# Kernel optimization log

Hardware: AMD Instinct MI355X
Metric: run time of the kernel (lower is better)

Reference implementation:

```python
import jax, jax.numpy as jnp
from jax import lax
import numpy as np

KW = 9
PAD = KW // 2  # 4, matches int(kernel_width/2) with stride-1 'same' conv


def _scnn_dir(x, w, b):
    """Sequential SCNN scan over axis 1 of x (shape [N, S, W, C]).
    Each step: cur = relu(conv1d_along_C(prev)) + x[:, i], out[0] = x[:, 0].
    conv is cross-correlation with kernel w (shape [KW]) + scalar bias b,
    matching nn.Conv2d(1, 1, kernel_size=(1, KW), padding=(0, PAD)).
    """
    k = w.reshape(1, 1, 1, KW)  # OIHW-style kernel: out=1, in=1, (1, KW)

    def conv(prev):  # prev: [N, W, C]
        y = lax.conv_general_dilated(prev[:, None, :, :], k,
                                     window_strides=(1, 1),
                                     padding=((0, 0), (PAD, PAD)))
        return y[:, 0] + b  # [N, W, C]

    xt = jnp.moveaxis(x, 1, 0)  # [S, N, W, C]

    def step(prev, xi):
        cur = jax.nn.relu(conv(prev)) + xi
        return cur, cur

    _, rest = lax.scan(step, xt[0], xt[1:])
    out = jnp.concatenate([xt[:1], rest], axis=0)
    return jnp.moveaxis(out, 0, 1)  # [N, S, W, C]


def setup_inputs() -> dict:
    key = jax.random.key(0)
    ks = jax.random.split(key, 9)
    N, C, H, W = 8, 128, 160, 160
    x = jax.random.normal(ks[0], (N, C, H, W), dtype=jnp.float32)
    scale = 1.0 / np.sqrt(KW)  # torch Conv2d default init scale (uniform bound)
    def wgt(k):
        return jax.random.uniform(k, (KW,), jnp.float32, -scale, scale)
    def bia(k):
        return jax.random.uniform(k, (), jnp.float32, -scale, scale)
    return {
        "x": x,
        "w_d": wgt(ks[1]), "b_d": bia(ks[2]),
        "w_u": wgt(ks[3]), "b_u": bia(ks[4]),
        "w_l": wgt(ks[5]), "b_l": bia(ks[6]),
        "w_r": wgt(ks[7]), "b_r": bia(ks[8]),
    }


def reference(x, w_d, b_d, w_u, b_u, w_l, b_l, w_r, b_r):
    out = jnp.transpose(x, (0, 2, 3, 1))                 # NCHW -> NHWC, scan over H (down)
    out = jax.nn.relu(_scnn_dir(out, w_d, b_d))
    out = jnp.flip(out, axis=1)                          # up direction
    out = jax.nn.relu(_scnn_dir(out, w_u, b_u))
    out = jnp.transpose(out, (0, 2, 1, 3))               # scan over W (left)
    out = jax.nn.relu(_scnn_dir(out, w_l, b_l))
    out = jnp.flip(out, axis=1)                          # right direction
    out = jax.nn.relu(_scnn_dir(out, w_r, b_r))
    return jnp.transpose(out, (0, 3, 2, 1))              # back to NCHW
```

## Files before the change

### kernel.cpp

```cpp
#include <hip/hip_runtime.h>

#define NB 8
#define CH 128
#define HH 160
#define WW 160
#define SPILL 100
#define LDS_ROWS 60

__device__ __forceinline__ float dpp_up1(float x) {
    return __int_as_float(__builtin_amdgcn_update_dpp(0, __float_as_int(x), 0x138, 0xF, 0xF, true));
}
__device__ __forceinline__ float dpp_dn1(float x) {
    return __int_as_float(__builtin_amdgcn_update_dpp(0, __float_as_int(x), 0x130, 0xF, 0xF, true));
}

__device__ __forceinline__ float2 conv9(float2 p, const float* w, float b) {
    float m1x = dpp_up1(p.x), m1y = dpp_up1(p.y);
    float m2x = dpp_up1(m1x), m2y = dpp_up1(m1y);
    float p1x = dpp_dn1(p.x), p1y = dpp_dn1(p.y);
    float p2x = dpp_dn1(p1x), p2y = dpp_dn1(p1y);
    float e0=m2x,e1=m2y,e2=m1x,e3=m1y,e4=p.x,e5=p.y,e6=p1x,e7=p1y,e8=p2x,e9=p2y;
    float ax = fmaf(w[0], e0, b);       ax = fmaf(w[3], e3, ax); ax = fmaf(w[6], e6, ax);
    float bx = w[1]*e1;                 bx = fmaf(w[4], e4, bx); bx = fmaf(w[7], e7, bx);
    float cx = w[2]*e2;                 cx = fmaf(w[5], e5, cx); cx = fmaf(w[8], e8, cx);
    float ay = fmaf(w[0], e1, b);       ay = fmaf(w[3], e4, ay); ay = fmaf(w[6], e7, ay);
    float by = w[1]*e2;                 by = fmaf(w[4], e5, by); by = fmaf(w[7], e8, by);
    float cy = w[2]*e3;                 cy = fmaf(w[5], e6, cy); cy = fmaf(w[8], e9, cy);
    return make_float2((ax + bx) + cx, (ay + by) + cy);
}

__global__ __launch_bounds__(256) void k0_transpose(const float* __restrict__ x,
                                                    float* __restrict__ A) {
    __shared__ float t[32][132];
    int p0 = blockIdx.x * 128;
    int c0 = blockIdx.y * 32;
    int n  = blockIdx.z;
    int tid = threadIdx.x;
    const float* xn = x + (size_t)n * CH * HH * WW;
    float* An = A + (size_t)n * HH * WW * CH;
    #pragma unroll
    for (int j = 0; j < 4; j++) {
        int c = j*8 + tid/32;
        int q4 = (tid%32)*4;
        float4 v = *(const float4*)(xn + (size_t)(c0 + c) * (HH*WW) + p0 + q4);
        *(float4*)&t[c][q4] = v;
    }
    __syncthreads();
    #pragma unroll
    for (int j = 0; j < 8; j++) {
        int p  = j*16 + tid/16;
        int cq = (tid%16)*2;
        float2 v = make_float2(t[cq][p], t[cq+1][p]);
        *(float2*)(An + (size_t)(p0 + p) * CH + c0 + cq) = v;
    }
}

__global__ __launch_bounds__(64) void k1_vert(float* __restrict__ A,
        const float* __restrict__ wdp, const float* __restrict__ bdp,
        const float* __restrict__ wup, const float* __restrict__ bup) {
    __shared__ float lds[LDS_ROWS][CH];
    int lane = threadIdx.x;
    int w = blockIdx.x, n = blockIdx.y;
    float wd[9], wu[9];
    #pragma unroll
    for (int j = 0; j < 9; j++) { wd[j] = wdp[j]; wu[j] = wup[j]; }
    float bd = bdp[0], bu = bup[0];
    float* col = A + ((size_t)n * HH * WW + w) * CH + 2*lane;
    const size_t RS = (size_t)WW * CH;

    float2 d;
    float2 qf[16];
    #pragma unroll
    for (int i = 0; i < 16; i++) qf[i] = *(const float2*)(col + (size_t)i * RS);
    for (int hb = 0; hb < HH; hb += 16) {
        #pragma unroll
        for (int k = 0; k < 16; k++) {
            int h = hb + k;
            float2 xr = qf[k];
            if (h + 16 < HH) qf[k] = *(const float2*)(col + (size_t)(h+16) * RS);
            if (h == 0) d = xr;
            else {
                float2 cv = conv9(d, wd, bd);
                d.x = fmaxf(cv.x, 0.f) + xr.x;
                d.y = fmaxf(cv.y, 0.f) + xr.y;
            }
            float rx = fmaxf(d.x, 0.f), ry = fmaxf(d.y, 0.f);
            if (h < SPILL) *(float2*)(col + (size_t)h * RS) = make_float2(rx, ry);
            else { lds[h-SPILL][lane] = rx; lds[h-SPILL][64+lane] = ry; }
        }
    }

    float2 u;
    float2 tf[8];
    #pragma unroll
    for (int k = 0; k < 8; k++) {
        int h = HH - 1 - k;
        tf[k] = make_float2(lds[h-SPILL][lane], lds[h-SPILL][64+lane]);
    }
    for (int sb = 0; sb < HH; sb += 8) {
        #pragma unroll
        for (int k = 0; k < 8; k++) {
            int s = sb + k;
            int h = HH - 1 - s;
            float2 t2 = tf[k];
            int h2 = h - 8;
            if (h2 >= SPILL)    tf[k] = make_float2(lds[h2-SPILL][lane], lds[h2-SPILL][64+lane]);
            else if (h2 >= 0)   tf[k] = *(const float2*)(col + (size_t)h2 * RS);
            if (s == 0) u = t2;
            else {
                float2 cv = conv9(u, wu, bu);
                u.x = fmaxf(cv.x, 0.f) + t2.x;
                u.y = fmaxf(cv.y, 0.f) + t2.y;
            }
            *(float2*)(col + (size_t)h * RS) = u;
        }
    }
}

__global__ __launch_bounds__(64) void k2_horz(float* __restrict__ A,
        const float* __restrict__ wlp, const float* __restrict__ blp,
        const float* __restrict__ wrp, const float* __restrict__ brp) {
    __shared__ float lds[LDS_ROWS][CH];
    int lane = threadIdx.x;
    int hp = blockIdx.x, n = blockIdx.y;
    float wl[9], wr[9];
    #pragma unroll
    for (int j = 0; j < 9; j++) { wl[j] = wlp[j]; wr[j] = wrp[j]; }
    float bl = blp[0], br = brp[0];
    float* row0 = A + ((size_t)n * HH + hp) * WW * CH + 2*lane;
    const size_t PS = CH;

    float2 l;
    float2 qf[16];
    #pragma unroll
    for (int i = 0; i < 16; i++) qf[i] = *(const float2*)(row0 + (size_t)i * PS);
    for (int ab = 0; ab < WW; ab += 16) {
        #pragma unroll
        for (int k = 0; k < 16; k++) {
            int a = ab + k;
            float2 xr = qf[k];
            if (a + 16 < WW) qf[k] = *(const float2*)(row0 + (size_t)(a+16) * PS);
            xr.x = fmaxf(xr.x, 0.f); xr.y = fmaxf(xr.y, 0.f);
            if (a == 0) l = xr;
            else {
                float2 cv = conv9(l, wl, bl);
                l.x = fmaxf(cv.x, 0.f) + xr.x;
                l.y = fmaxf(cv.y, 0.f) + xr.y;
            }
            float rx = fmaxf(l.x, 0.f), ry = fmaxf(l.y, 0.f);
            if (a < SPILL) *(float2*)(row0 + (size_t)a * PS) = make_float2(rx, ry);
            else { lds[a-SPILL][lane] = rx; lds[a-SPILL][64+lane] = ry; }
        }
    }

    float2 r;
    float2 tf[8];
    #pragma unroll
    for (int k = 0; k < 8; k++) {
        int a = WW - 1 - k;
        tf[k] = make_float2(lds[a-SPILL][lane], lds[a-SPILL][64+lane]);
    }
    for (int sb = 0; sb < WW; sb += 8) {
        #pragma unroll
        for (int k = 0; k < 8; k++) {
            int s = sb + k;
            int a = WW - 1 - s;
            float2 t6 = tf[k];
            int a2 = a - 8;
            if (a2 >= SPILL)    tf[k] = make_float2(lds[a2-SPILL][lane], lds[a2-SPILL][64+lane]);
            else if (a2 >= 0)   tf[k] = *(const float2*)(row0 + (size_t)a2 * PS);
            if (s == 0) r = t6;
            else {
                float2 cv = conv9(r, wr, br);
                r.x = fmaxf(cv.x, 0.f) + t6.x;
                r.y = fmaxf(cv.y, 0.f) + t6.y;
            }
            *(float2*)(row0 + (size_t)a * PS) = r;
        }
    }
}

__global__ __launch_bounds__(256) void k3_out(const float* __restrict__ A,
                                              float* __restrict__ out) {
    __shared__ float t[32][132];
    int w0 = blockIdx.x * 32;
    int nh = blockIdx.y;
    int n = nh / HH, h = nh % HH;
    const float* Ap = A + (size_t)nh * WW * CH;
    int tid = threadIdx.x;
    #pragma unroll
    for (int j = 0; j < 4; j++) {
        int wl = j*8 + tid/32;
        int c4 = (tid%32)*4;
        float4 v = *(const float4*)(Ap + (size_t)(w0 + wl) * CH + c4);
        v.x = fmaxf(v.x, 0.f); v.y = fmaxf(v.y, 0.f);
        v.z = fmaxf(v.z, 0.f); v.w = fmaxf(v.w, 0.f);
        *(float4*)&t[wl][c4] = v;
    }
    __syncthreads();
    int ho = HH - 1 - h;
    #pragma unroll
    for (int j = 0; j < 16; j++) {
        int c  = j*8 + tid/32;
        int wl = tid%32;
        out[((size_t)(n * CH + c) * HH + ho) * WW + (WW - 1 - (w0 + wl))] = t[wl][c];
    }
}

extern "C" void kernel_launch(void* const* d_in, const int* in_sizes, int n_in,
                              void* d_out, int out_size, void* d_ws, size_t ws_size,
                              hipStream_t stream) {
    (void)in_sizes; (void)n_in; (void)out_size; (void)ws_size;
    const float* x  = (const float*)d_in[0];
    const float* wd = (const float*)d_in[1];
    const float* bd = (const float*)d_in[2];
    const float* wu = (const float*)d_in[3];
    const float* bu = (const float*)d_in[4];
    const float* wl = (const float*)d_in[5];
    const float* bl = (const float*)d_in[6];
    const float* wr = (const float*)d_in[7];
    const float* br = (const float*)d_in[8];
    float* out = (float*)d_out;
    float* A   = (float*)d_ws;

    dim3 g0(HH*WW/128, CH/32, NB), b0(256);
    k0_transpose<<<g0, b0, 0, stream>>>(x, A);

    dim3 g1(WW, NB), b1(64);
    k1_vert<<<g1, b1, 0, stream>>>(A, wd, bd, wu, bu);

    dim3 g2(HH, NB);
    k2_horz<<<g2, b1, 0, stream>>>(A, wl, bl, wr, br);

    dim3 g3(WW/32, NB*HH), b3(256);
    k3_out<<<g3, b3, 0, stream>>>(A, out);
}
```

Measured before the change: 362.5 us.

## Fuse output transpose into horizontal scan via swizzled LDS ring buffer

```diff
diff --git a/kernel.cpp b/kernel.cpp
--- a/kernel.cpp
+++ b/kernel.cpp
@@ -91,19 +91,19 @@
     }
 
     float2 u;
-    float2 tf[8];
-    #pragma unroll
-    for (int k = 0; k < 8; k++) {
+    float2 tf[16];
+    #pragma unroll
+    for (int k = 0; k < 16; k++) {
         int h = HH - 1 - k;
         tf[k] = make_float2(lds[h-SPILL][lane], lds[h-SPILL][64+lane]);
     }
-    for (int sb = 0; sb < HH; sb += 8) {
-        #pragma unroll
-        for (int k = 0; k < 8; k++) {
+    for (int sb = 0; sb < HH; sb += 16) {
+        #pragma unroll
+        for (int k = 0; k < 16; k++) {
             int s = sb + k;
             int h = HH - 1 - s;
             float2 t2 = tf[k];
-            int h2 = h - 8;
+            int h2 = h - 16;
             if (h2 >= SPILL)    tf[k] = make_float2(lds[h2-SPILL][lane], lds[h2-SPILL][64+lane]);
             else if (h2 >= 0)   tf[k] = *(const float2*)(col + (size_t)h2 * RS);
             if (s == 0) u = t2;
@@ -119,7 +119,8 @@
 
 __global__ __launch_bounds__(64) void k2_horz(float* __restrict__ A,
         const float* __restrict__ wlp, const float* __restrict__ blp,
-        const float* __restrict__ wrp, const float* __restrict__ brp) {
+        const float* __restrict__ wrp, const float* __restrict__ brp,
+        float* __restrict__ out) {
     __shared__ float lds[LDS_ROWS][CH];
     int lane = threadIdx.x;
     int hp = blockIdx.x, n = blockIdx.y;
@@ -149,61 +150,69 @@
             }
             float rx = fmaxf(l.x, 0.f), ry = fmaxf(l.y, 0.f);
             if (a < SPILL) *(float2*)(row0 + (size_t)a * PS) = make_float2(rx, ry);
-            else { lds[a-SPILL][lane] = rx; lds[a-SPILL][64+lane] = ry; }
-        }
-    }
-
-    float2 r;
-    float2 tf[8];
-    #pragma unroll
-    for (int k = 0; k < 8; k++) {
+            else {
+                int r = a - SPILL;
+                int sw = r & 31;
+                lds[r][lane ^ sw] = rx;
+                lds[r][64 + (lane ^ sw)] = ry;
+            }
+        }
+    }
+
+    float2 u;
+    float2 tf[16];
+    #pragma unroll
+    for (int k = 0; k < 16; k++) {
         int a = WW - 1 - k;
-        tf[k] = make_float2(lds[a-SPILL][lane], lds[a-SPILL][64+lane]);
-    }
-    for (int sb = 0; sb < WW; sb += 8) {
-        #pragma unroll
-        for (int k = 0; k < 8; k++) {
-            int s = sb + k;
+        int r = a - SPILL;
+        int sw = r & 31;
+        tf[k] = make_float2(lds[r][lane ^ sw], lds[r][64 + (lane ^ sw)]);
+    }
+    int ho  = HH - 1 - hp;
+    int l31 = lane & 31;
+    int hi  = lane >> 5;
+    float* ob = out + ((size_t)(n * CH + hi) * HH + ho) * WW + l31;
+    int jf = (179 - l31) % 60;
+    int js = 59;
+
+    for (int sb = 0; sb < WW; sb += 32) {
+        #pragma unroll
+        for (int kk = 0; kk < 32; kk++) {
+            int s = sb + kk;
             int a = WW - 1 - s;
-            float2 t6 = tf[k];
-            int a2 = a - 8;
-            if (a2 >= SPILL)    tf[k] = make_float2(lds[a2-SPILL][lane], lds[a2-SPILL][64+lane]);
-            else if (a2 >= 0)   tf[k] = *(const float2*)(row0 + (size_t)a2 * PS);
-            if (s == 0) r = t6;
-            else {
-                float2 cv = conv9(r, wr, br);
-                r.x = fmaxf(cv.x, 0.f) + t6.x;
-                r.y = fmaxf(cv.y, 0.f) + t6.y;
-            }
-            *(float2*)(row0 + (size_t)a * PS) = r;
-        }
-    }
-}
-
-__global__ __launch_bounds__(256) void k3_out(const float* __restrict__ A,
-                                              float* __restrict__ out) {
-    __shared__ float t[32][132];
-    int w0 = blockIdx.x * 32;
-    int nh = blockIdx.y;
-    int n = nh / HH, h = nh % HH;
-    const float* Ap = A + (size_t)nh * WW * CH;
-    int tid = threadIdx.x;
-    #pragma unroll
-    for (int j = 0; j < 4; j++) {
-        int wl = j*8 + tid/32;
-        int c4 = (tid%32)*4;
-        float4 v = *(const float4*)(Ap + (size_t)(w0 + wl) * CH + c4);
-        v.x = fmaxf(v.x, 0.f); v.y = fmaxf(v.y, 0.f);
-        v.z = fmaxf(v.z, 0.f); v.w = fmaxf(v.w, 0.f);
-        *(float4*)&t[wl][c4] = v;
-    }
-    __syncthreads();
-    int ho = HH - 1 - h;
-    #pragma unroll
-    for (int j = 0; j < 16; j++) {
-        int c  = j*8 + tid/32;
-        int wl = tid%32;
-        out[((size_t)(n * CH + c) * HH + ho) * WW + (WW - 1 - (w0 + wl))] = t[wl][c];
+            float2 t6 = tf[kk & 15];
+            int a2 = a - 16;
+            if (a2 >= SPILL) {
+                int r = a2 - SPILL;
+                int sw = r & 31;
+                tf[kk & 15] = make_float2(lds[r][lane ^ sw], lds[r][64 + (lane ^ sw)]);
+            } else if (a2 >= 0) {
+                tf[kk & 15] = *(const float2*)(row0 + (size_t)a2 * PS);
+            }
+            if (s == 0) u = t6;
+            else {
+                float2 cv = conv9(u, wr, br);
+                u.x = fmaxf(cv.x, 0.f) + t6.x;
+                u.y = fmaxf(cv.y, 0.f) + t6.y;
+            }
+            {
+                int sw = js & 31;
+                lds[js][lane ^ sw]        = fmaxf(u.x, 0.f);
+                lds[js][64 + (lane ^ sw)] = fmaxf(u.y, 0.f);
+            }
+            js = js ? js - 1 : 59;
+        }
+        {
+            int jx = jf & 31;
+            int pl = jf * 128 + (hi << 6);
+            const float* lp = &lds[0][0];
+            #pragma unroll
+            for (int i = 0; i < 64; i++) {
+                float v = lp[pl + (i ^ jx)];
+                ob[(size_t)(2*i) * (HH*WW) + sb] = v;
+            }
+            jf -= 32; if (jf < 0) jf += 60;
+        }
     }
 }
 
@@ -230,8 +239,5 @@
     k1_vert<<<g1, b1, 0, stream>>>(A, wd, bd, wu, bu);
 
     dim3 g2(HH, NB);
-    k2_horz<<<g2, b1, 0, stream>>>(A, wl, bl, wr, br);
-
-    dim3 g3(WW/32, NB*HH), b3(256);
-    k3_out<<<g3, b3, 0, stream>>>(A, out);
-}
+    k2_horz<<<g2, b1, 0, stream>>>(A, wl, bl, wr, br, out);
+}
```

Result: faster. 332.1 us (-8.4%).
